# Performance work log

Measured on AMD Instinct MI355X. Metric: run time of the kernel, lower is better.

## Reference

```python
import jax, jax.numpy as jnp
import numpy as np
from jax import lax

EPS = 1e-12  # torch F.normalize eps


def _l2norm(x):
    n = jnp.linalg.norm(x, axis=-1, keepdims=True)
    return x / jnp.maximum(n, EPS)


def _conv1x1(x, w):
    # x: [B,C,H,W], w: [O,C] (1x1 conv, no bias)
    return jnp.einsum('bchw,oc->bohw', x, w)


def _se(x, w1, w2):
    # AdaptiveAvgPool2d(1) -> 1x1 conv (no bias) -> ReLU -> 1x1 conv (no bias) -> ReLU
    p = jnp.mean(x, axis=(2, 3))                      # [B,256]
    h = jax.nn.relu(jnp.einsum('bc,oc->bo', p, w1))   # [B,320]
    return jax.nn.relu(jnp.einsum('bc,oc->bo', h, w2))  # [B,1280]


def _tdec(x, wk_w, wk_b, wv_w, wv_b, red_w, rise_w, rise_b):
    # fc_reduce: 1x1 conv 256->128
    x1 = _conv1x1(x, red_w)                           # [B,128,H,W]
    B, d, H, W = x1.shape
    t = x1.reshape(B, d, H * W).transpose(0, 2, 1)    # [B,N,128] tokens
    # same WK linear produces both q and k (xq == xk in the source)
    k = _l2norm(jnp.einsum('bnd,ed->bne', t, wk_w) + wk_b)  # [B,N,128]
    v = _l2norm(jnp.einsum('bnd,ed->bne', t, wv_w) + wv_b)  # [B,N,128]
    # bmm(wq[B,d,N], wk[B,N,d]) -> [B,d,d] channel gram, temp 30 softmax
    attn = jax.nn.softmax(jnp.einsum('bni,bnj->bij', k, k) * 30.0, axis=-1)
    # bmm(attn[B,d,d], v^T[B,d,N]) -> [B,d,N], reshape back to map
    ot = jnp.einsum('bij,bnj->bin', attn, v).reshape(B, d, H, W)
    return _conv1x1(ot, rise_w) + rise_b[None, :, None, None]


def _fwd(x0, x1, x2, x3, x4, spec_w1, spec_w2, comm_w1, comm_w2,
         pre_w, pre_b, wk1_w, wk1_b, wv1_w, wv1_b, red1_w, rise1_w, rise1_b,
         wk2_w, wk2_b, wv2_w, wv2_b, red2_w, rise2_w, rise2_b):
    xs = jnp.stack([x0, x1, x2, x3, x4])              # [5,B,256,H,W]
    B = x0.shape[0]
    # reduce(lambda x,y: abs(x-y), down_x)
    diff = x0
    for xi in (x1, x2, x3, x4):
        diff = jnp.abs(diff - xi)
    ssum = xs.sum(axis=0)
    wd = jax.nn.softmax(_se(diff, spec_w1, spec_w2).reshape(B, 5, 256), axis=1)
    ws = jax.nn.softmax(_se(ssum, comm_w1, comm_w2).reshape(B, 5, 256), axis=1)
    # v2[i] = x_i*wd_i + x_i*ws_i + x_i ; v3 = sum_i v2[i]
    v3 = jnp.einsum('sbchw,bsc->bchw', xs, wd + ws + 1.0)
    pre = jax.nn.relu(
        lax.conv_general_dilated(v3, pre_w, (1, 1), ((1, 1), (1, 1)),
                                 dimension_numbers=('NCHW', 'OIHW', 'NCHW'))
        + pre_b[None, :, None, None])
    f1 = _tdec(pre, wk1_w, wk1_b, wv1_w, wv1_b, red1_w, rise1_w, rise1_b)
    f3 = _tdec(f1 + v3, wk2_w, wk2_b, wv2_w, wv2_b, red2_w, rise2_w, rise2_b)
    return f1 + f3 + v3


def setup_inputs() -> dict:
    key = jax.random.key(0)
    ks = iter(jax.random.split(key, 40))
    B, C, H, W = 16, 256, 64, 64

    def p(shape, scale=0.05):
        return jax.random.normal(next(ks), shape, jnp.float32) * scale

    inp = {f'x{i}': jax.random.normal(next(ks), (B, C, H, W), jnp.float32) for i in range(5)}
    inp.update(
        spec_w1=p((320, 256)), spec_w2=p((1280, 320)),
        comm_w1=p((320, 256)), comm_w2=p((1280, 320)),
        pre_w=p((256, 256, 3, 3)), pre_b=p((256,)),
        wk1_w=p((128, 128)), wk1_b=p((128,)), wv1_w=p((128, 128)), wv1_b=p((128,)),
        red1_w=p((128, 256)), rise1_w=p((256, 128)), rise1_b=p((256,)),
        wk2_w=p((128, 128)), wk2_b=p((128,)), wv2_w=p((128, 128)), wv2_b=p((128,)),
        red2_w=p((128, 256)), rise2_w=p((256, 128)), rise2_b=p((256,)),
    )
    return inp


def reference(x0, x1, x2, x3, x4, spec_w1, spec_w2, comm_w1, comm_w2,
              pre_w, pre_b, wk1_w, wk1_b, wv1_w, wv1_b, red1_w, rise1_w, rise1_b,
              wk2_w, wk2_b, wv2_w, wv2_b, red2_w, rise2_w, rise2_b):
    return _fwd(x0, x1, x2, x3, x4, spec_w1, spec_w2, comm_w1, comm_w2,
                pre_w, pre_b, wk1_w, wk1_b, wv1_w, wv1_b, red1_w, rise1_w, rise1_b,
                wk2_w, wk2_b, wv2_w, wv2_b, red2_w, rise2_w, rise2_b)
```

## Files before the change

### kernel.cpp

```cpp
#include <hip/hip_runtime.h>

#define DI __device__ __forceinline__

typedef short s16x8 __attribute__((ext_vector_type(8)));
typedef unsigned short u16;
typedef u16 u16x4 __attribute__((ext_vector_type(4)));
typedef u16 u16x8 __attribute__((ext_vector_type(8)));
typedef u16 u16x16 __attribute__((ext_vector_type(16)));
typedef float f32x4 __attribute__((ext_vector_type(4)));
typedef _Float16 f16;
typedef f16 f16x4 __attribute__((ext_vector_type(4)));

DI float bf2f(u16 v) { return __builtin_bit_cast(float, (unsigned)v << 16); }
DI u16 f2bf(float f) {
  unsigned u = __builtin_bit_cast(unsigned, f);
  return (u16)((u + 0x7fffu + ((u >> 16) & 1u)) >> 16);
}

__global__ void k_cast8(u16* __restrict__ dst,
    const float* __restrict__ s0, const float* __restrict__ s1,
    const float* __restrict__ s2, const float* __restrict__ s3,
    const float* __restrict__ s4, const float* __restrict__ s5,
    const float* __restrict__ s6, const float* __restrict__ s7) {
  int i = blockIdx.x * 256 + threadIdx.x;
  const float* src; int base;
  if (i < 32768) { src = s0; base = 0; }
  else if (i < 49152) { src = s1; base = 32768; }
  else if (i < 65536) { src = s2; base = 49152; }
  else if (i < 98304) { src = s3; base = 65536; }
  else if (i < 131072) { src = s4; base = 98304; }
  else if (i < 147456) { src = s5; base = 131072; }
  else if (i < 163840) { src = s6; base = 147456; }
  else { src = s7; base = 163840; }
  dst[i] = f2bf(src[i - base]);
}

__global__ void k_wconv(u16* __restrict__ dst, const float* __restrict__ src) {
  int i = blockIdx.x * 256 + threadIdx.x;
  if (i < 9 * 256 * 256) {
    int tap = i >> 16, rem = i & 65535;
    dst[i] = f2bf(src[(size_t)rem * 9 + tap]);
  }
}

__global__ __launch_bounds__(256) void k_pool(
    const float* __restrict__ x0, const float* __restrict__ x1,
    const float* __restrict__ x2, const float* __restrict__ x3,
    const float* __restrict__ x4, float* __restrict__ pd, float* __restrict__ ps,
    f16* __restrict__ hx1, f16* __restrict__ hx2,
    f16* __restrict__ hx3, f16* __restrict__ hx4) {
  int c = blockIdx.x, b = blockIdx.y;
  size_t ebase = ((size_t)b * 256 + c) * 4096 + threadIdx.x * 4;
  float sd = 0.f, sm = 0.f;
#pragma unroll
  for (int it = 0; it < 4; ++it) {
    size_t off = ebase + it * 1024;
    f32x4 a0 = *(const f32x4*)(x0 + off);
    f32x4 a1 = *(const f32x4*)(x1 + off);
    f32x4 a2 = *(const f32x4*)(x2 + off);
    f32x4 a3 = *(const f32x4*)(x3 + off);
    f32x4 a4 = *(const f32x4*)(x4 + off);
    f16x4 h1, h2, h3, h4;
#pragma unroll
    for (int e = 0; e < 4; ++e) {
      float d = fabsf(a0[e] - a1[e]); d = fabsf(d - a2[e]); d = fabsf(d - a3[e]); d = fabsf(d - a4[e]);
      sd += d; sm += a0[e] + a1[e] + a2[e] + a3[e] + a4[e];
      h1[e] = (f16)a1[e]; h2[e] = (f16)a2[e]; h3[e] = (f16)a3[e]; h4[e] = (f16)a4[e];
    }
    *(f16x4*)(hx1 + off) = h1;
    *(f16x4*)(hx2 + off) = h2;
    *(f16x4*)(hx3 + off) = h3;
    *(f16x4*)(hx4 + off) = h4;
  }
  for (int o = 32; o; o >>= 1) { sd += __shfl_xor(sd, o); sm += __shfl_xor(sm, o); }
  __shared__ float rb[4][2];
  int wv = threadIdx.x >> 6, lane = threadIdx.x & 63;
  if (!lane) { rb[wv][0] = sd; rb[wv][1] = sm; }
  __syncthreads();
  if (!threadIdx.x) {
    float a = rb[0][0] + rb[1][0] + rb[2][0] + rb[3][0];
    float s2 = rb[0][1] + rb[1][1] + rb[2][1] + rb[3][1];
    pd[b * 256 + c] = a * (1.f / 4096.f);
    ps[b * 256 + c] = s2 * (1.f / 4096.f);
  }
}

__global__ __launch_bounds__(256) void k_se1(
    const float* __restrict__ pd, const float* __restrict__ ps,
    const float* __restrict__ sw1, const float* __restrict__ cw1,
    float* __restrict__ h1) {
  int b = blockIdx.y, z = blockIdx.z;
  int wv = threadIdx.x >> 6, lane = threadIdx.x & 63;
  int e = blockIdx.x * 4 + wv;
  const float* in = (z ? ps : pd) + b * 256;
  const float* w = (z ? cw1 : sw1) + (size_t)e * 256;
  float a = 0.f;
#pragma unroll
  for (int i = 0; i < 4; ++i) a += in[lane + 64 * i] * w[lane + 64 * i];
  for (int o = 32; o; o >>= 1) a += __shfl_xor(a, o);
  if (!lane) h1[((size_t)z * 16 + b) * 320 + e] = fmaxf(a, 0.f);
}

__global__ __launch_bounds__(256) void k_se2(
    const float* __restrict__ h1, const float* __restrict__ sw2,
    const float* __restrict__ cw2, float* __restrict__ h2) {
  int b = blockIdx.y, z = blockIdx.z;
  int wv = threadIdx.x >> 6, lane = threadIdx.x & 63;
  int e = blockIdx.x * 4 + wv;
  const float* in = h1 + ((size_t)z * 16 + b) * 320;
  const float* w = (z ? cw2 : sw2) + (size_t)e * 320;
  float a = 0.f;
#pragma unroll
  for (int i = 0; i < 5; ++i) a += in[lane + 64 * i] * w[lane + 64 * i];
  for (int o = 32; o; o >>= 1) a += __shfl_xor(a, o);
  if (!lane) h2[((size_t)z * 16 + b) * 1280 + e] = fmaxf(a, 0.f);
}

__global__ __launch_bounds__(256) void k_se3(
    const float* __restrict__ h2, float* __restrict__ wt) {
  int b = blockIdx.x, t = threadIdx.x;
  const float* Hs = h2 + (size_t)b * 1280;
  const float* Hc = h2 + (size_t)(16 + b) * 1280;
  float d0 = Hs[t], d1 = Hs[256 + t], d2 = Hs[512 + t], d3 = Hs[768 + t], d4 = Hs[1024 + t];
  float m = fmaxf(fmaxf(fmaxf(d0, d1), fmaxf(d2, d3)), d4);
  float e0 = expf(d0 - m), e1 = expf(d1 - m), e2 = expf(d2 - m), e3 = expf(d3 - m), e4 = expf(d4 - m);
  float inv = 1.f / (e0 + e1 + e2 + e3 + e4);
  float c0 = Hc[t], c1 = Hc[256 + t], c2 = Hc[512 + t], c3 = Hc[768 + t], c4 = Hc[1024 + t];
  float mc = fmaxf(fmaxf(fmaxf(c0, c1), fmaxf(c2, c3)), c4);
  float g0 = expf(c0 - mc), g1 = expf(c1 - mc), g2 = expf(c2 - mc), g3 = expf(c3 - mc), g4 = expf(c4 - mc);
  float ci = 1.f / (g0 + g1 + g2 + g3 + g4);
  size_t base = (size_t)b * 1280 + t;
  wt[base + 0 * 256] = e0 * inv + g0 * ci + 1.f;
  wt[base + 1 * 256] = e1 * inv + g1 * ci + 1.f;
  wt[base + 2 * 256] = e2 * inv + g2 * ci + 1.f;
  wt[base + 3 * 256] = e3 * inv + g3 * ci + 1.f;
  wt[base + 4 * 256] = e4 * inv + g4 * ci + 1.f;
}

__global__ __launch_bounds__(256) void k_v3(
    const float* __restrict__ x0, const f16* __restrict__ hx1,
    const f16* __restrict__ hx2, const f16* __restrict__ hx3,
    const f16* __restrict__ hx4, const float* __restrict__ wt,
    u16* __restrict__ v3b) {
  int h = blockIdx.x, b = blockIdx.y;
  __shared__ float W[1280];
  __shared__ u16 T[256][68];
  int t = threadIdx.x;
  for (int s = t; s < 1280; s += 256) W[s] = wt[(size_t)b * 1280 + s];
  __syncthreads();
  int csub = t >> 4, l16 = t & 15;
  size_t ebase = (size_t)b * 256 * 4096 + h * 64 + l16 * 4;
#pragma unroll 4
  for (int ci = 0; ci < 16; ++ci) {
    int c = ci * 16 + csub;
    size_t a = ebase + (size_t)c * 4096;
    f32x4 v0 = *(const f32x4*)(x0 + a);
    f16x4 v1 = *(const f16x4*)(hx1 + a);
    f16x4 v2 = *(const f16x4*)(hx2 + a);
    f16x4 v3 = *(const f16x4*)(hx3 + a);
    f16x4 v4 = *(const f16x4*)(hx4 + a);
    float w0 = W[c], w1 = W[256 + c], w2 = W[512 + c], w3 = W[768 + c], w4 = W[1024 + c];
    u16x4 ov;
#pragma unroll
    for (int e = 0; e < 4; ++e)
      ov[e] = f2bf(v0[e] * w0 + (float)v1[e] * w1 + (float)v2[e] * w2 +
                   (float)v3[e] * w3 + (float)v4[e] * w4);
    *(u16x4*)(&T[c][l16 * 4]) = ov;
  }
  __syncthreads();
  int w = t >> 2, oct = t & 3;
  size_t obase = ((size_t)b * 4096 + h * 64 + w) * 256;
  for (int pass = 0; pass < 8; ++pass) {
    int c0 = oct * 8 + pass * 32;
    u16x8 ov;
#pragma unroll
    for (int jj = 0; jj < 8; ++jj) ov[jj] = T[c0 + jj][w];
    *(u16x8*)(v3b + obase + c0) = ov;
  }
}

__global__ __launch_bounds__(256) void k_conv(
    const u16* __restrict__ v3b, const u16* __restrict__ Wt,
    const float* __restrict__ bias, u16* __restrict__ pre) {
  int o = blockIdx.x;
  int wg = (o & 7) * 128 + (o >> 3);
  int oh = wg & 1, hp = (wg >> 1) & 31, b = wg >> 6;
  __shared__ __align__(16) u16 Ain[4 * 64 * 40];
  __shared__ __align__(16) u16 Bls[2][128 * 40];
  int t = threadIdx.x, wv = t >> 6, lane = t & 63;
  int wm = (wv >> 1) * 64, wn = (wv & 1) * 64, fr = lane & 15, ko = lane >> 4;

  auto loadA = [&](int cc, int s) -> u16x16 {
    int r = s >> 7, rest = s & 127, w = rest >> 1, half = rest & 1;
    int hs = hp * 2 - 1 + r;
    u16x16 v = {};
    if ((unsigned)hs < 64u)
      v = *(const u16x16*)(v3b + (((size_t)b * 64 + hs) * 64 + w) * 256 + cc * 32 + half * 16);
    return v;
  };
  auto storeA = [&](int s, u16x16 v) {
    int r = s >> 7, rest = s & 127, w = rest >> 1, half = rest & 1;
    *(u16x16*)(Ain + (r * 64 + w) * 40 + half * 16) = v;
  };
  auto loadB = [&](int tap, int cc) -> u16x16 {
    int n = t >> 1, half = t & 1;
    return *(const u16x16*)(Wt + ((size_t)tap * 256 + oh * 128 + n) * 256 + cc * 32 + half * 16);
  };
  auto storeB = [&](int bsel, u16x16 v) {
    int n = t >> 1, half = t & 1;
    *(u16x16*)(Bls[bsel] + n * 40 + half * 16) = v;
  };

  u16x16 pA0 = loadA(0, t), pA1 = loadA(0, t + 256);
  u16x16 rB = loadB(0, 0);
  storeA(t, pA0); storeA(t + 256, pA1); storeB(0, rB);
  rB = loadB(1, 0);
  __syncthreads();

  f32x4 acc[4][4] = {};
  int buf = 0;
  for (int cc = 0; cc < 8; ++cc) {
#pragma unroll
    for (int tap = 0; tap < 9; ++tap) {
      const int dh = tap / 3 - 1, dw = tap % 3 - 1;
      s16x8 af[4], bfr[4];
#pragma unroll
      for (int i = 0; i < 4; ++i) {
        int m = wm + i * 16 + fr, r = m >> 6, wq = m & 63;
        int wqd = wq + dw;
        s16x8 v = {};
        if ((unsigned)wqd < 64u)
          v = *(const s16x8*)(Ain + ((r + dh + 1) * 64 + wqd) * 40 + ko * 8);
        af[i] = v;
      }
#pragma unroll
      for (int j = 0; j < 4; ++j)
        bfr[j] = *(const s16x8*)(Bls[buf] + (wn + j * 16 + fr) * 40 + ko * 8);
#pragma unroll
      for (int i = 0; i < 4; ++i)
#pragma unroll
        for (int j = 0; j < 4; ++j)
          acc[i][j] = __builtin_amdgcn_mfma_f32_16x16x32_bf16(af[i], bfr[j], acc[i][j], 0, 0, 0);
      const int u = cc * 9 + tap;
      if (u < 71) {
        if (tap == 8) {
          __syncthreads();
          storeA(t, pA0); storeA(t + 256, pA1);
        }
        storeB(buf ^ 1, rB);
        if (u + 2 <= 71) {
          const int un = u + 2;
          rB = loadB(un % 9, un / 9);
        }
        if (tap == 7 && cc < 7) { pA0 = loadA(cc + 1, t); pA1 = loadA(cc + 1, t + 256); }
        __syncthreads();
        buf ^= 1;
      }
    }
  }
#pragma unroll
  for (int i = 0; i < 4; ++i) {
    int m0 = wm + i * 16 + ko * 4;
#pragma unroll
    for (int j = 0; j < 4; ++j) {
      int och = oh * 128 + wn + j * 16 + fr;
      float bv = bias[och];
#pragma unroll
      for (int r = 0; r < 4; ++r) {
        float v = fmaxf(acc[i][j][r] + bv, 0.f);
        pre[((size_t)b * 4096 + hp * 128 + m0 + r) * 256 + och] = f2bf(v);
      }
    }
  }
}

__global__ __launch_bounds__(256) void k_qkv(
    const u16* __restrict__ in,
    const u16* __restrict__ redW,
    const u16* __restrict__ wkW,
    const u16* __restrict__ wvW,
    const float* __restrict__ kb, const float* __restrict__ vb,
    u16* __restrict__ vout,
    float* __restrict__ gp) {
  int nt = blockIdx.x, b = blockIdx.y;
  const u16* Ab = in + ((size_t)b * 4096 + nt * 128) * 256;
  __shared__ __align__(16) u16 Ald[128 * 40];
  __shared__ __align__(16) u16 Bld[128 * 40];
  __shared__ __align__(16) u16 T[128 * 136];
  __shared__ float SS[2][128];
  int t = threadIdx.x, wv = t >> 6, lane = t & 63;
  int wm = (wv >> 1) * 64, wn = (wv & 1) * 64, fr = lane & 15, ko = lane >> 4;
  f32x4 acc[4][4] = {};
  for (int kc = 0; kc < 256; kc += 32) {
    for (int s = t; s < 512; s += 256) {
      int r = s >> 2, ks = s & 3;
      *(u16x8*)(Ald + r * 40 + ks * 8) = *(const u16x8*)(Ab + (size_t)r * 256 + kc + ks * 8);
    }
    for (int s = t; s < 512; s += 256) {
      int r = s >> 2, ks = s & 3;
      *(u16x8*)(Bld + r * 40 + ks * 8) = *(const u16x8*)(redW + (size_t)r * 256 + kc + ks * 8);
    }
    __syncthreads();
    s16x8 af[4], bf[4];
#pragma unroll
    for (int i = 0; i < 4; ++i) af[i] = *(const s16x8*)(Ald + (wm + i * 16 + fr) * 40 + ko * 8);
#pragma unroll
    for (int j = 0; j < 4; ++j) bf[j] = *(const s16x8*)(Bld + (wn + j * 16 + fr) * 40 + ko * 8);
#pragma unroll
    for (int i = 0; i < 4; ++i)
#pragma unroll
      for (int j = 0; j < 4; ++j)
        acc[i][j] = __builtin_amdgcn_mfma_f32_16x16x32_bf16(af[i], bf[j], acc[i][j], 0, 0, 0);
    __syncthreads();
  }
#pragma unroll
  for (int i = 0; i < 4; ++i)
#pragma unroll
    for (int j = 0; j < 4; ++j)
#pragma unroll
      for (int r = 0; r < 4; ++r)
        T[(wm + i * 16 + ko * 4 + r) * 136 + wn + j * 16 + fr] = f2bf(acc[i][j][r]);

  for (int z = 0; z < 2; ++z) {
    const u16* W = z ? wkW : wvW;
    const float* bias = z ? kb : vb;
    f32x4 a2[4][4] = {};
#pragma unroll
    for (int h = 0; h < 2; ++h) {
      __syncthreads();
      for (int s = t; s < 512; s += 256) {
        int r = s >> 2, ks = s & 3;
        *(u16x8*)(Ald + r * 40 + ks * 8) = *(const u16x8*)(W + (size_t)r * 128 + h * 64 + ks * 8);
      }
      for (int s = t; s < 512; s += 256) {
        int r = s >> 2, ks = s & 3;
        *(u16x8*)(Bld + r * 40 + ks * 8) = *(const u16x8*)(W + (size_t)r * 128 + h * 64 + 32 + ks * 8);
      }
      __syncthreads();
#pragma unroll
      for (int kk = 0; kk < 2; ++kk) {
        const u16* Bsrc = kk ? Bld : Ald;
        s16x8 af[4], bf[4];
#pragma unroll
        for (int i = 0; i < 4; ++i)
          af[i] = *(const s16x8*)(T + (size_t)(wm + i * 16 + fr) * 136 + h * 64 + kk * 32 + ko * 8);
#pragma unroll
        for (int j = 0; j < 4; ++j)
          bf[j] = *(const s16x8*)(Bsrc + (wn + j * 16 + fr) * 40 + ko * 8);
#pragma unroll
        for (int i = 0; i < 4; ++i)
#pragma unroll
          for (int j = 0; j < 4; ++j)
            a2[i][j] = __builtin_amdgcn_mfma_f32_16x16x32_bf16(af[i], bf[j], a2[i][j], 0, 0, 0);
      }
    }
    float bj[4];
#pragma unroll
    for (int j = 0; j < 4; ++j) bj[j] = bias[wn + j * 16 + fr];
    float pss[4][4];
#pragma unroll
    for (int i = 0; i < 4; ++i)
#pragma unroll
      for (int r = 0; r < 4; ++r) pss[i][r] = 0.f;
#pragma unroll
    for (int i = 0; i < 4; ++i)
#pragma unroll
      for (int j = 0; j < 4; ++j)
#pragma unroll
        for (int r = 0; r < 4; ++r) {
          float v = a2[i][j][r] + bj[j];
          a2[i][j][r] = v;
          pss[i][r] += v * v;
        }
#pragma unroll
    for (int m = 1; m < 16; m <<= 1)
#pragma unroll
      for (int i = 0; i < 4; ++i)
#pragma unroll
        for (int r = 0; r < 4; ++r) pss[i][r] += __shfl_xor(pss[i][r], m);
    if (fr == 0)
#pragma unroll
      for (int i = 0; i < 4; ++i)
#pragma unroll
        for (int r = 0; r < 4; ++r) SS[wv & 1][wm + i * 16 + ko * 4 + r] = pss[i][r];
    __syncthreads();
    float sc[4][4];
#pragma unroll
    for (int i = 0; i < 4; ++i)
#pragma unroll
      for (int r = 0; r < 4; ++r) {
        int tok = wm + i * 16 + ko * 4 + r;
        float s2 = SS[0][tok] + SS[1][tok];
        sc[i][r] = 1.f / fmaxf(sqrtf(s2), 1e-12f);
      }
#pragma unroll
    for (int i = 0; i < 4; ++i)
#pragma unroll
      for (int j = 0; j < 4; ++j)
#pragma unroll
        for (int r = 0; r < 4; ++r) a2[i][j][r] *= sc[i][r];
    if (z == 0) {
      size_t tokbase = (size_t)b * 4096 + nt * 128;
#pragma unroll
      for (int i = 0; i < 4; ++i)
#pragma unroll
        for (int j = 0; j < 4; ++j) {
          u16* dst = vout + (tokbase + wm + i * 16 + ko * 4) * 128 + wn + j * 16 + fr;
#pragma unroll
          for (int r = 0; r < 4; ++r) dst[(size_t)r * 128] = f2bf(a2[i][j][r]);
        }
    } else {
#pragma unroll
      for (int i = 0; i < 4; ++i)
#pragma unroll
        for (int j = 0; j < 4; ++j)
#pragma unroll
          for (int r = 0; r < 4; ++r)
            T[(size_t)(wn + j * 16 + fr) * 136 + wm + i * 16 + ko * 4 + r] = f2bf(a2[i][j][r]);
      __syncthreads();
      f32x4 g3[4][4] = {};
      for (int kc = 0; kc < 128; kc += 32) {
        s16x8 af[4], bf[4];
#pragma unroll
        for (int i = 0; i < 4; ++i)
          af[i] = *(const s16x8*)(T + (size_t)(wm + i * 16 + fr) * 136 + kc + ko * 8);
#pragma unroll
        for (int j = 0; j < 4; ++j)
          bf[j] = *(const s16x8*)(T + (size_t)(wn + j * 16 + fr) * 136 + kc + ko * 8);
#pragma unroll
        for (int i = 0; i < 4; ++i)
#pragma unroll
          for (int j = 0; j < 4; ++j)
            g3[i][j] = __builtin_amdgcn_mfma_f32_16x16x32_bf16(af[i], bf[j], g3[i][j], 0, 0, 0);
      }
      float* dst = gp + ((size_t)(b * 32 + nt)) * 16384;
#pragma unroll
      for (int i = 0; i < 4; ++i) {
        int m0 = wm + i * 16 + ko * 4;
#pragma unroll
        for (int j = 0; j < 4; ++j) {
          int nc = wn + j * 16 + fr;
#pragma unroll
          for (int r = 0; r < 4; ++r) dst[(size_t)(m0 + r) * 128 + nc] = g3[i][j][r];
        }
      }
    }
  }
}

template <int MODE>
__global__ __launch_bounds__(256) void k_pvrise(
    const u16* __restrict__ vbuf,
    const u16* __restrict__ attnb,
    const u16* __restrict__ riseW,
    const float* __restrict__ bias,
    const u16* __restrict__ add0, const u16* __restrict__ add1,
    u16* __restrict__ out0, u16* __restrict__ out1, float* __restrict__ outf) {
  int nt = blockIdx.x, b = blockIdx.y;
  const u16* Ab = vbuf + ((size_t)b * 4096 + nt * 128) * 128;
  const u16* Bb = attnb + (size_t)b * 128 * 128;
  __shared__ __align__(16) u16 Ald[128 * 40];
  __shared__ __align__(16) u16 Bld[128 * 40];
  __shared__ __align__(16) u16 T[128 * 136];
  int t = threadIdx.x, wv = t >> 6, lane = t & 63;
  int wm = (wv >> 1) * 64, wn = (wv & 1) * 64, fr = lane & 15, ko = lane >> 4;
  f32x4 acc[4][4] = {};
  for (int kc = 0; kc < 128; kc += 32) {
    for (int s = t; s < 512; s += 256) {
      int r = s >> 2, ks = s & 3;
      *(u16x8*)(Ald + r * 40 + ks * 8) = *(const u16x8*)(Ab + (size_t)r * 128 + kc + ks * 8);
    }
    for (int s = t; s < 512; s += 256) {
      int r = s >> 2, ks = s & 3;
      *(u16x8*)(Bld + r * 40 + ks * 8) = *(const u16x8*)(Bb + (size_t)r * 128 + kc + ks * 8);
    }
    __syncthreads();
    s16x8 af[4], bf[4];
#pragma unroll
    for (int i = 0; i < 4; ++i) af[i] = *(const s16x8*)(Ald + (wm + i * 16 + fr) * 40 + ko * 8);
#pragma unroll
    for (int j = 0; j < 4; ++j) bf[j] = *(const s16x8*)(Bld + (wn + j * 16 + fr) * 40 + ko * 8);
#pragma unroll
    for (int i = 0; i < 4; ++i)
#pragma unroll
      for (int j = 0; j < 4; ++j)
        acc[i][j] = __builtin_amdgcn_mfma_f32_16x16x32_bf16(af[i], bf[j], acc[i][j], 0, 0, 0);
    __syncthreads();
  }
#pragma unroll
  for (int i = 0; i < 4; ++i)
#pragma unroll
    for (int j = 0; j < 4; ++j)
#pragma unroll
      for (int r = 0; r < 4; ++r)
        T[(wm + i * 16 + ko * 4 + r) * 136 + wn + j * 16 + fr] = f2bf(acc[i][j][r]);

  size_t tokbase = (size_t)b * 4096 + nt * 128;
  for (int z = 0; z < 2; ++z) {
    const u16* W = riseW + (size_t)z * 128 * 128;
    f32x4 a2[4][4] = {};
#pragma unroll
    for (int h = 0; h < 2; ++h) {
      __syncthreads();
      for (int s = t; s < 512; s += 256) {
        int r = s >> 2, ks = s & 3;
        *(u16x8*)(Ald + r * 40 + ks * 8) = *(const u16x8*)(W + (size_t)r * 128 + h * 64 + ks * 8);
      }
      for (int s = t; s < 512; s += 256) {
        int r = s >> 2, ks = s & 3;
        *(u16x8*)(Bld + r * 40 + ks * 8) = *(const u16x8*)(W + (size_t)r * 128 + h * 64 + 32 + ks * 8);
      }
      __syncthreads();
#pragma unroll
      for (int kk = 0; kk < 2; ++kk) {
        const u16* Bsrc = kk ? Bld : Ald;
        s16x8 af[4], bf[4];
#pragma unroll
        for (int i = 0; i < 4; ++i)
          af[i] = *(const s16x8*)(T + (size_t)(wm + i * 16 + fr) * 136 + h * 64 + kk * 32 + ko * 8);
#pragma unroll
        for (int j = 0; j < 4; ++j)
          bf[j] = *(const s16x8*)(Bsrc + (wn + j * 16 + fr) * 40 + ko * 8);
#pragma unroll
        for (int i = 0; i < 4; ++i)
#pragma unroll
          for (int j = 0; j < 4; ++j)
            a2[i][j] = __builtin_amdgcn_mfma_f32_16x16x32_bf16(af[i], bf[j], a2[i][j], 0, 0, 0);
      }
    }
#pragma unroll
    for (int i = 0; i < 4; ++i) {
      int m0 = wm + i * 16 + ko * 4;
#pragma unroll
      for (int j = 0; j < 4; ++j) {
        int o = z * 128 + wn + j * 16 + fr;
        float bv = bias[o];
        size_t idx = (tokbase + m0) * 256 + o;
        if constexpr (MODE == 3) {
#pragma unroll
          for (int r = 0; r < 4; ++r) {
            float f1v = a2[i][j][r] + bv;
            out0[idx + (size_t)r * 256] = f2bf(f1v);
            out1[idx + (size_t)r * 256] = f2bf(f1v + bf2f(add0[idx + (size_t)r * 256]));
          }
        } else {
          f32x4 vv;
#pragma unroll
          for (int r = 0; r < 4; ++r)
            vv[r] = a2[i][j][r] + bv + bf2f(add0[idx + (size_t)r * 256]) +
                    bf2f(add1[idx + (size_t)r * 256]);
          *(f32x4*)(outf + ((size_t)b * 256 + o) * 4096 + nt * 128 + m0) = vv;
        }
      }
    }
  }
}

__global__ void k_soft(const float* __restrict__ gp, u16* __restrict__ attn) {
  int i = blockIdx.x, b = blockIdx.y, l = threadIdx.x;
  float s0 = 0.f, s1 = 0.f;
  for (int ks = 0; ks < 32; ++ks) {
    const float* row = gp + ((size_t)(b * 32 + ks)) * 16384 + (size_t)i * 128;
    s0 += row[l]; s1 += row[l + 64];
  }
  s0 *= 30.f; s1 *= 30.f;
  float m = fmaxf(s0, s1);
  for (int o = 32; o; o >>= 1) m = fmaxf(m, __shfl_xor(m, o));
  float e0 = expf(s0 - m), e1 = expf(s1 - m);
  float s = e0 + e1;
  for (int o = 32; o; o >>= 1) s += __shfl_xor(s, o);
  float inv = 1.f / s;
  u16* dst = attn + ((size_t)b * 128 + i) * 128;
  dst[l] = f2bf(e0 * inv);
  dst[l + 64] = f2bf(e1 * inv);
}

extern "C" void kernel_launch(void* const* d_in, const int* in_sizes, int n_in,
                              void* d_out, int out_size, void* d_ws, size_t ws_size,
                              hipStream_t stream) {
  (void)in_sizes; (void)n_in; (void)out_size; (void)ws_size;
  const float* x0 = (const float*)d_in[0];
  const float* x1 = (const float*)d_in[1];
  const float* x2 = (const float*)d_in[2];
  const float* x3 = (const float*)d_in[3];
  const float* x4 = (const float*)d_in[4];
  const float* spec_w1 = (const float*)d_in[5];
  const float* spec_w2 = (const float*)d_in[6];
  const float* comm_w1 = (const float*)d_in[7];
  const float* comm_w2 = (const float*)d_in[8];
  const float* pre_w = (const float*)d_in[9];
  const float* pre_bias = (const float*)d_in[10];
  const float* wk1_w = (const float*)d_in[11];
  const float* wk1_b = (const float*)d_in[12];
  const float* wv1_w = (const float*)d_in[13];
  const float* wv1_b = (const float*)d_in[14];
  const float* red1_w = (const float*)d_in[15];
  const float* rise1_w = (const float*)d_in[16];
  const float* rise1_b = (const float*)d_in[17];
  const float* wk2_w = (const float*)d_in[18];
  const float* wk2_b = (const float*)d_in[19];
  const float* wv2_w = (const float*)d_in[20];
  const float* wv2_b = (const float*)d_in[21];
  const float* red2_w = (const float*)d_in[22];
  const float* rise2_w = (const float*)d_in[23];
  const float* rise2_b = (const float*)d_in[24];
  float* out = (float*)d_out;

  char* wsp = (char*)d_ws;
  size_t off = 0;
  auto alloc = [&](size_t bytes) -> void* {
    off = (off + 255) & ~(size_t)255;
    void* p = wsp + off;
    off += bytes;
    return p;
  };
  float* pd = (float*)alloc(16 * 256 * 4);
  float* ps = (float*)alloc(16 * 256 * 4);
  float* h1b = (float*)alloc(2 * 16 * 320 * 4);
  float* h2b = (float*)alloc(2 * 16 * 1280 * 4);
  float* wtb = (float*)alloc(16 * 5 * 256 * 4);
  u16* v3b = (u16*)alloc((size_t)16 * 4096 * 256 * 2);
  u16* Wtc = (u16*)alloc((size_t)9 * 256 * 256 * 2);
  u16* wall = (u16*)alloc((size_t)196608 * 2);
  u16* red1b = wall;
  u16* wk1b = wall + 32768;
  u16* wv1b = wall + 49152;
  u16* rise1b = wall + 65536;
  u16* red2b = wall + 98304;
  u16* wk2b = wall + 131072;
  u16* wv2b = wall + 147456;
  u16* rise2b = wall + 163840;
  u16* pre = (u16*)alloc((size_t)16 * 4096 * 256 * 2);
  float* gpart = (float*)alloc((size_t)16 * 32 * 128 * 128 * 4);
  u16* vbuf = (u16*)alloc((size_t)16 * 4096 * 128 * 2);
  u16* attn = (u16*)alloc((size_t)16 * 128 * 128 * 2);
  u16* spacer = (u16*)alloc((size_t)16 * 4096 * 128 * 2);
  u16* f1b = (u16*)alloc((size_t)16 * 4096 * 256 * 2);
  (void)spacer;
  u16* in2b = pre;
  f16* hx = (f16*)pre;
  const size_t HXN = (size_t)16 * 256 * 4096;
  f16* hx1 = hx;
  f16* hx2 = hx + HXN;
  f16* hx3 = hx + 2 * HXN;
  f16* hx4 = hx + 3 * HXN;

  k_cast8<<<dim3(768), 256, 0, stream>>>(wall, red1_w, wk1_w, wv1_w, rise1_w,
                                         red2_w, wk2_w, wv2_w, rise2_w);
  k_wconv<<<dim3(2304), 256, 0, stream>>>(Wtc, pre_w);

  k_pool<<<dim3(256, 16), 256, 0, stream>>>(x0, x1, x2, x3, x4, pd, ps, hx1, hx2, hx3, hx4);
  k_se1<<<dim3(80, 16, 2), 256, 0, stream>>>(pd, ps, spec_w1, comm_w1, h1b);
  k_se2<<<dim3(320, 16, 2), 256, 0, stream>>>(h1b, spec_w2, comm_w2, h2b);
  k_se3<<<dim3(16), 256, 0, stream>>>(h2b, wtb);
  k_v3<<<dim3(64, 16), 256, 0, stream>>>(x0, hx1, hx2, hx3, hx4, wtb, v3b);
  k_conv<<<dim3(1024), 256, 0, stream>>>(v3b, Wtc, pre_bias, pre);

  k_qkv<<<dim3(32, 16), 256, 0, stream>>>(pre, red1b, wk1b, wv1b, wk1_b, wv1_b, vbuf, gpart);
  k_soft<<<dim3(128, 16), 64, 0, stream>>>(gpart, attn);
  k_pvrise<3><<<dim3(32, 16), 256, 0, stream>>>(vbuf, attn, rise1b, rise1_b,
      v3b, nullptr, f1b, in2b, nullptr);

  k_qkv<<<dim3(32, 16), 256, 0, stream>>>(in2b, red2b, wk2b, wv2b, wk2_b, wv2_b, vbuf, gpart);
  k_soft<<<dim3(128, 16), 64, 0, stream>>>(gpart, attn);
  k_pvrise<4><<<dim3(32, 16), 256, 0, stream>>>(vbuf, attn, rise2b, rise2_b,
      f1b, v3b, nullptr, nullptr, out);
}
```

Baseline: 437.4 us.

## Merge weight-cast kernels, fold SE softmax into v3, deepen conv B prefetch

Combines the two weight-conversion kernels into one launch and folds the per-batch SE softmax (k_se3) into k_v3, which now computes the blend weights directly into shared memory. This removes two kernel launches and the intermediate weight buffer. The conv kernel also prefetches B tiles two steps ahead instead of one, to hide global load latency, at the cost of extra registers. Each of the 64 k_v3 blocks per batch recomputes the small softmax redundantly.

```diff
diff --git a/kernel.cpp b/kernel.cpp
--- a/kernel.cpp
+++ b/kernel.cpp
@@ -17,29 +17,28 @@
   return (u16)((u + 0x7fffu + ((u >> 16) & 1u)) >> 16);
 }
 
-__global__ void k_cast8(u16* __restrict__ dst,
+__global__ void k_prep(u16* __restrict__ wall,
     const float* __restrict__ s0, const float* __restrict__ s1,
     const float* __restrict__ s2, const float* __restrict__ s3,
     const float* __restrict__ s4, const float* __restrict__ s5,
-    const float* __restrict__ s6, const float* __restrict__ s7) {
+    const float* __restrict__ s6, const float* __restrict__ s7,
+    u16* __restrict__ Wtc, const float* __restrict__ pre_w) {
   int i = blockIdx.x * 256 + threadIdx.x;
-  const float* src; int base;
-  if (i < 32768) { src = s0; base = 0; }
-  else if (i < 49152) { src = s1; base = 32768; }
-  else if (i < 65536) { src = s2; base = 49152; }
-  else if (i < 98304) { src = s3; base = 65536; }
-  else if (i < 131072) { src = s4; base = 98304; }
-  else if (i < 147456) { src = s5; base = 131072; }
-  else if (i < 163840) { src = s6; base = 147456; }
-  else { src = s7; base = 163840; }
-  dst[i] = f2bf(src[i - base]);
-}
-
-__global__ void k_wconv(u16* __restrict__ dst, const float* __restrict__ src) {
-  int i = blockIdx.x * 256 + threadIdx.x;
-  if (i < 9 * 256 * 256) {
-    int tap = i >> 16, rem = i & 65535;
-    dst[i] = f2bf(src[(size_t)rem * 9 + tap]);
+  if (i < 196608) {
+    const float* src; int base;
+    if (i < 32768) { src = s0; base = 0; }
+    else if (i < 49152) { src = s1; base = 32768; }
+    else if (i < 65536) { src = s2; base = 49152; }
+    else if (i < 98304) { src = s3; base = 65536; }
+    else if (i < 131072) { src = s4; base = 98304; }
+    else if (i < 147456) { src = s5; base = 131072; }
+    else if (i < 163840) { src = s6; base = 147456; }
+    else { src = s7; base = 163840; }
+    wall[i] = f2bf(src[i - base]);
+  } else {
+    int j = i - 196608;
+    int tap = j >> 16, rem = j & 65535;
+    Wtc[j] = f2bf(pre_w[(size_t)rem * 9 + tap]);
   }
 }
 
@@ -116,37 +115,32 @@
   if (!lane) h2[((size_t)z * 16 + b) * 1280 + e] = fmaxf(a, 0.f);
 }
 
-__global__ __launch_bounds__(256) void k_se3(
-    const float* __restrict__ h2, float* __restrict__ wt) {
-  int b = blockIdx.x, t = threadIdx.x;
-  const float* Hs = h2 + (size_t)b * 1280;
-  const float* Hc = h2 + (size_t)(16 + b) * 1280;
-  float d0 = Hs[t], d1 = Hs[256 + t], d2 = Hs[512 + t], d3 = Hs[768 + t], d4 = Hs[1024 + t];
-  float m = fmaxf(fmaxf(fmaxf(d0, d1), fmaxf(d2, d3)), d4);
-  float e0 = expf(d0 - m), e1 = expf(d1 - m), e2 = expf(d2 - m), e3 = expf(d3 - m), e4 = expf(d4 - m);
-  float inv = 1.f / (e0 + e1 + e2 + e3 + e4);
-  float c0 = Hc[t], c1 = Hc[256 + t], c2 = Hc[512 + t], c3 = Hc[768 + t], c4 = Hc[1024 + t];
-  float mc = fmaxf(fmaxf(fmaxf(c0, c1), fmaxf(c2, c3)), c4);
-  float g0 = expf(c0 - mc), g1 = expf(c1 - mc), g2 = expf(c2 - mc), g3 = expf(c3 - mc), g4 = expf(c4 - mc);
-  float ci = 1.f / (g0 + g1 + g2 + g3 + g4);
-  size_t base = (size_t)b * 1280 + t;
-  wt[base + 0 * 256] = e0 * inv + g0 * ci + 1.f;
-  wt[base + 1 * 256] = e1 * inv + g1 * ci + 1.f;
-  wt[base + 2 * 256] = e2 * inv + g2 * ci + 1.f;
-  wt[base + 3 * 256] = e3 * inv + g3 * ci + 1.f;
-  wt[base + 4 * 256] = e4 * inv + g4 * ci + 1.f;
-}
-
 __global__ __launch_bounds__(256) void k_v3(
     const float* __restrict__ x0, const f16* __restrict__ hx1,
     const f16* __restrict__ hx2, const f16* __restrict__ hx3,
-    const f16* __restrict__ hx4, const float* __restrict__ wt,
+    const f16* __restrict__ hx4, const float* __restrict__ h2b,
     u16* __restrict__ v3b) {
   int h = blockIdx.x, b = blockIdx.y;
   __shared__ float W[1280];
   __shared__ u16 T[256][68];
   int t = threadIdx.x;
-  for (int s = t; s < 1280; s += 256) W[s] = wt[(size_t)b * 1280 + s];
+  {
+    const float* Hs = h2b + (size_t)b * 1280;
+    const float* Hc = h2b + (size_t)(16 + b) * 1280;
+    float d0 = Hs[t], d1 = Hs[256 + t], d2 = Hs[512 + t], d3 = Hs[768 + t], d4 = Hs[1024 + t];
+    float m = fmaxf(fmaxf(fmaxf(d0, d1), fmaxf(d2, d3)), d4);
+    float e0 = expf(d0 - m), e1 = expf(d1 - m), e2 = expf(d2 - m), e3 = expf(d3 - m), e4 = expf(d4 - m);
+    float inv = 1.f / (e0 + e1 + e2 + e3 + e4);
+    float c0 = Hc[t], c1 = Hc[256 + t], c2 = Hc[512 + t], c3 = Hc[768 + t], c4 = Hc[1024 + t];
+    float mc = fmaxf(fmaxf(fmaxf(c0, c1), fmaxf(c2, c3)), c4);
+    float g0 = expf(c0 - mc), g1 = expf(c1 - mc), g2 = expf(c2 - mc), g3 = expf(c3 - mc), g4 = expf(c4 - mc);
+    float ci = 1.f / (g0 + g1 + g2 + g3 + g4);
+    W[t] = e0 * inv + g0 * ci + 1.f;
+    W[256 + t] = e1 * inv + g1 * ci + 1.f;
+    W[512 + t] = e2 * inv + g2 * ci + 1.f;
+    W[768 + t] = e3 * inv + g3 * ci + 1.f;
+    W[1024 + t] = e4 * inv + g4 * ci + 1.f;
+  }
   __syncthreads();
   int csub = t >> 4, l16 = t & 15;
   size_t ebase = (size_t)b * 256 * 4096 + h * 64 + l16 * 4;
@@ -212,9 +206,10 @@
   };
 
   u16x16 pA0 = loadA(0, t), pA1 = loadA(0, t + 256);
-  u16x16 rB = loadB(0, 0);
-  storeA(t, pA0); storeA(t + 256, pA1); storeB(0, rB);
-  rB = loadB(1, 0);
+  u16x16 rB0 = loadB(0, 0);
+  storeA(t, pA0); storeA(t + 256, pA1); storeB(0, rB0);
+  rB0 = loadB(1, 0);
+  u16x16 rB1 = loadB(2, 0);
   __syncthreads();
 
   f32x4 acc[4][4] = {};
@@ -247,10 +242,11 @@
           __syncthreads();
           storeA(t, pA0); storeA(t + 256, pA1);
         }
-        storeB(buf ^ 1, rB);
-        if (u + 2 <= 71) {
-          const int un = u + 2;
-          rB = loadB(un % 9, un / 9);
+        storeB(buf ^ 1, rB0);
+        rB0 = rB1;
+        if (u + 3 <= 71) {
+          const int un = u + 3;
+          rB1 = loadB(un % 9, un / 9);
         }
         if (tap == 7 && cc < 7) { pA0 = loadA(cc + 1, t); pA1 = loadA(cc + 1, t + 256); }
         __syncthreads();
@@ -618,7 +614,6 @@
   float* ps = (float*)alloc(16 * 256 * 4);
   float* h1b = (float*)alloc(2 * 16 * 320 * 4);
   float* h2b = (float*)alloc(2 * 16 * 1280 * 4);
-  float* wtb = (float*)alloc(16 * 5 * 256 * 4);
   u16* v3b = (u16*)alloc((size_t)16 * 4096 * 256 * 2);
   u16* Wtc = (u16*)alloc((size_t)9 * 256 * 256 * 2);
   u16* wall = (u16*)alloc((size_t)196608 * 2);
@@ -645,15 +640,13 @@
   f16* hx3 = hx + 2 * HXN;
   f16* hx4 = hx + 3 * HXN;
 
-  k_cast8<<<dim3(768), 256, 0, stream>>>(wall, red1_w, wk1_w, wv1_w, rise1_w,
-                                         red2_w, wk2_w, wv2_w, rise2_w);
-  k_wconv<<<dim3(2304), 256, 0, stream>>>(Wtc, pre_w);
+  k_prep<<<dim3(3072), 256, 0, stream>>>(wall, red1_w, wk1_w, wv1_w, rise1_w,
+                                         red2_w, wk2_w, wv2_w, rise2_w, Wtc, pre_w);
 
   k_pool<<<dim3(256, 16), 256, 0, stream>>>(x0, x1, x2, x3, x4, pd, ps, hx1, hx2, hx3, hx4);
   k_se1<<<dim3(80, 16, 2), 256, 0, stream>>>(pd, ps, spec_w1, comm_w1, h1b);
   k_se2<<<dim3(320, 16, 2), 256, 0, stream>>>(h1b, spec_w2, comm_w2, h2b);
-  k_se3<<<dim3(16), 256, 0, stream>>>(h2b, wtb);
-  k_v3<<<dim3(64, 16), 256, 0, stream>>>(x0, hx1, hx2, hx3, hx4, wtb, v3b);
+  k_v3<<<dim3(64, 16), 256, 0, stream>>>(x0, hx1, hx2, hx3, hx4, h2b, v3b);
   k_conv<<<dim3(1024), 256, 0, stream>>>(v3b, Wtc, pre_bias, pre);
 
   k_qkv<<<dim3(32, 16), 256, 0, stream>>>(pre, red1b, wk1b, wv1b, wk1_b, wv1_b, vbuf, gpart);
```

Result: slower. 454.3 us (+3.9%).
